# Performance work log

Measured on AMD Instinct MI355X. Metric: run time of the kernel, lower is better.

The kernel has to match this reference:

```python
import jax, jax.numpy as jnp
import numpy as np

B, C, G, N_OBJ = 256, 1019, 7, 16
IMG_SIZE = 448.0

def setup_inputs() -> dict:
    key = jax.random.key(0)
    k1, k2, k3, k4 = jax.random.split(key, 4)
    outputs = jax.random.normal(k1, (B, 5 + C, G, G), dtype=jnp.float32)
    boxes = jax.random.uniform(k2, (B, N_OBJ, 4), dtype=jnp.float32, minval=0.0, maxval=IMG_SIZE)
    labels = jax.random.randint(k3, (B, N_OBJ), 1, C + 1, dtype=jnp.int32)  # 1..C (code uses label-1)
    coords = jax.random.randint(k4, (B, N_OBJ, 2), 0, G, dtype=jnp.int32)   # (x, y) grid cells
    # objectness target matrix: 1.0 at cells containing an object, else 0 (soft CE target)
    bidx = jnp.arange(B)[:, None]
    obj = jnp.zeros((B, G, G), jnp.float32).at[bidx, coords[..., 1], coords[..., 0]].set(1.0)
    obj_matrix = obj.reshape(B, G * G)
    return {"outputs": outputs, "boxes": boxes, "labels": labels, "coords": coords, "obj_matrix": obj_matrix}

def reference(outputs, boxes, labels, coords, obj_matrix):
    Bn = outputs.shape[0]
    # objectness CE with soft targets: mean over batch of -sum(target * log_softmax(pred))
    p_obj = outputs[:, 0].reshape(Bn, -1)                      # [B, 49]
    cel_obj = jnp.mean(-jnp.sum(obj_matrix * jax.nn.log_softmax(p_obj, axis=-1), axis=-1))
    # gather per-object predictions at grid cells (x=coords[...,0], y=coords[...,1])
    bidx = jnp.arange(Bn)[:, None]
    y = coords[..., 1]
    x = coords[..., 0]
    pred_boxes = outputs[:, 1:5][bidx, :, y, x]                # [B, N_OBJ, 4]
    tgt_scaled = jnp.round(boxes / IMG_SIZE * 10.0) / 10.0     # np.round(x/IMG_SIZE, 1)
    bb_loss = jnp.sum((tgt_scaled - pred_boxes) ** 2) / Bn
    # per-object class cross-entropy, summed then divided by batch
    pred_labels = outputs[:, 5:][bidx, :, y, x]                # [B, N_OBJ, C]
    logp = jax.nn.log_softmax(pred_labels, axis=-1)
    ce = -jnp.take_along_axis(logp, (labels - 1)[..., None].astype(jnp.int32), axis=-1)
    cel_class = jnp.sum(ce) / Bn
    return cel_obj + bb_loss + cel_class
```

## Files before the change

### kernel.cpp

```cpp
#include <hip/hip_runtime.h>

#define BATCH 256
#define NCLS  1019
#define GRID  7
#define NOBJ  16
#define PLANE 49
#define NCH   1024
#define SLAB  (NCH * PLANE)
#define TPB   1024
#define NWAVE 16
#define NGRP  16

__global__ __launch_bounds__(TPB) void yolo_loss_kernel(
    const float* __restrict__ outputs,
    const float* __restrict__ boxes,
    const int*   __restrict__ labels,
    const int*   __restrict__ coords,
    const float* __restrict__ obj_matrix,
    float* __restrict__ out)
{
    const int b    = blockIdx.x;
    const int t    = threadIdx.x;
    const int lane = t & 63;
    const int w    = t >> 6;

    __shared__ float s_slot[NWAVE][4 * PLANE];
    __shared__ float s_sum[PLANE];
    __shared__ int   s_pos[NOBJ];
    __shared__ int   s_cl[NOBJ];
    __shared__ float s_red;

    const float*  ob  = outputs + (size_t)b * SLAB;
    const float4* ob4 = (const float4*)ob;

    if (t == 0) s_red = 0.0f;
    if (t < NOBJ) {
        int x = coords[(b * NOBJ + t) * 2 + 0];
        int y = coords[(b * NOBJ + t) * 2 + 1];
        s_pos[t] = y * GRID + x;
        s_cl[t]  = labels[b * NOBJ + t] - 1;
    }
    __syncthreads();

    if (w == 1) {
        float l = (lane < PLANE) ? ob[lane] : 0.0f;
        float s = (lane < PLANE) ? __expf(l) : 0.0f;
#pragma unroll
        for (int off = 32; off > 0; off >>= 1)
            s += __shfl_xor(s, off, 64);
        float lse = __logf(s);
        float mm = (lane < PLANE) ? obj_matrix[b * PLANE + lane] : 0.0f;
        float contrib = (lane < PLANE) ? -mm * (l - lse) : 0.0f;
#pragma unroll
        for (int off = 32; off > 0; off >>= 1)
            contrib += __shfl_xor(contrib, off, 64);
        if (lane == 0) atomicAdd(&s_red, contrib);
    }

    if (w == 2) {
        int o = lane >> 2, k = lane & 3;
        float pred = ob[(size_t)(1 + k) * PLANE + s_pos[o]];
        float tb   = boxes[(b * NOBJ + o) * 4 + k];
        float tgt  = rintf(tb * (10.0f / 448.0f)) * 0.1f;
        float d    = tgt - pred;
        float sq   = d * d;
#pragma unroll
        for (int off = 32; off > 0; off >>= 1)
            sq += __shfl_xor(sq, off, 64);
        if (lane == 0) atomicAdd(&s_red, sq);
    }

    const bool act = lane < PLANE;
    const int  lc  = act ? lane : 0;

    const float4* base = ob4 + (size_t)PLANE * w + lc;
    float4 v[NGRP];
#pragma unroll
    for (int i = 0; i < NGRP; ++i)
        v[i] = base[(size_t)PLANE * NWAVE * i];

    float a0 = 0.0f, a1 = 0.0f, a2 = 0.0f, a3 = 0.0f;
#pragma unroll
    for (int i = 0; i < NGRP; ++i) {
        a0 += __expf(v[i].x);
        a1 += __expf(v[i].y);
        a2 += __expf(v[i].z);
        a3 += __expf(v[i].w);
    }
    if (act) {
        float4* dst = (float4*)&s_slot[w][4 * lc];
        *dst = make_float4(a0, a1, a2, a3);
    }
    __syncthreads();

    if (w == 0 && lane < PLANE) {
        float s = 0.0f;
#pragma unroll
        for (int ww = 0; ww < NWAVE; ++ww) {
#pragma unroll
            for (int k = 0; k < 4; ++k)
                s += s_slot[ww][lane + PLANE * k];
        }
        float corr = 0.0f;
#pragma unroll
        for (int r = 0; r < 5; ++r)
            corr += __expf(ob[r * PLANE + lane]);
        s_sum[lane] = s - corr;
    }
    __syncthreads();

    if (w == 0 && lane < NOBJ) {
        float se = s_sum[s_pos[lane]];
        float tl = ob[(size_t)(5 + s_cl[lane]) * PLANE + s_pos[lane]];
        float ce = __logf(se) - tl;
        atomicAdd(&s_red, ce);
    }
    __syncthreads();

    if (t == 0) atomicAdd(out, s_red * (1.0f / (float)BATCH));
}

extern "C" void kernel_launch(void* const* d_in, const int* in_sizes, int n_in,
                              void* d_out, int out_size, void* d_ws, size_t ws_size,
                              hipStream_t stream) {
    const float* outputs    = (const float*)d_in[0];
    const float* boxes      = (const float*)d_in[1];
    const int*   labels     = (const int*)d_in[2];
    const int*   coords     = (const int*)d_in[3];
    const float* obj_matrix = (const float*)d_in[4];
    float* out = (float*)d_out;

    hipMemsetAsync(out, 0, sizeof(float), stream);
    yolo_loss_kernel<<<BATCH, TPB, 0, stream>>>(outputs, boxes, labels, coords,
                                                obj_matrix, out);
}
```

Baseline: 91.85 us.

## Split loss into two kernels, halving per-block channel work for more parallelism

The single per-batch kernel becomes two. The first kernel launches two blocks per batch item, each summing exponentials over half the channels and writing partial sums to workspace. The second kernel, small and with 128 threads, handles objectness CE, box loss and class CE using those partial sums. The memset is replaced by the first kernel zeroing the output. This doubles the block count so more CUs are busy on the 256-CU device, at the cost of a second launch and a workspace round trip.

```diff
diff --git a/kernel.cpp b/kernel.cpp
--- a/kernel.cpp
+++ b/kernel.cpp
@@ -7,73 +7,30 @@
 #define PLANE 49
 #define NCH   1024
 #define SLAB  (NCH * PLANE)
-#define TPB   1024
 #define NWAVE 16
-#define NGRP  16
+#define NGRP  8
 
-__global__ __launch_bounds__(TPB) void yolo_loss_kernel(
+__global__ __launch_bounds__(1024, 8) void yolo_sumexp_k1(
     const float* __restrict__ outputs,
-    const float* __restrict__ boxes,
-    const int*   __restrict__ labels,
-    const int*   __restrict__ coords,
-    const float* __restrict__ obj_matrix,
+    float* __restrict__ ws,
     float* __restrict__ out)
 {
-    const int b    = blockIdx.x;
+    const int blk  = blockIdx.x;
+    const int b    = blk >> 1;
+    const int h    = blk & 1;
     const int t    = threadIdx.x;
     const int lane = t & 63;
     const int w    = t >> 6;
 
+    if (blk == 0 && t == 0) out[0] = 0.0f;
+
     __shared__ float s_slot[NWAVE][4 * PLANE];
-    __shared__ float s_sum[PLANE];
-    __shared__ int   s_pos[NOBJ];
-    __shared__ int   s_cl[NOBJ];
-    __shared__ float s_red;
 
-    const float*  ob  = outputs + (size_t)b * SLAB;
-    const float4* ob4 = (const float4*)ob;
-
-    if (t == 0) s_red = 0.0f;
-    if (t < NOBJ) {
-        int x = coords[(b * NOBJ + t) * 2 + 0];
-        int y = coords[(b * NOBJ + t) * 2 + 1];
-        s_pos[t] = y * GRID + x;
-        s_cl[t]  = labels[b * NOBJ + t] - 1;
-    }
-    __syncthreads();
-
-    if (w == 1) {
-        float l = (lane < PLANE) ? ob[lane] : 0.0f;
-        float s = (lane < PLANE) ? __expf(l) : 0.0f;
-#pragma unroll
-        for (int off = 32; off > 0; off >>= 1)
-            s += __shfl_xor(s, off, 64);
-        float lse = __logf(s);
-        float mm = (lane < PLANE) ? obj_matrix[b * PLANE + lane] : 0.0f;
-        float contrib = (lane < PLANE) ? -mm * (l - lse) : 0.0f;
-#pragma unroll
-        for (int off = 32; off > 0; off >>= 1)
-            contrib += __shfl_xor(contrib, off, 64);
-        if (lane == 0) atomicAdd(&s_red, contrib);
-    }
-
-    if (w == 2) {
-        int o = lane >> 2, k = lane & 3;
-        float pred = ob[(size_t)(1 + k) * PLANE + s_pos[o]];
-        float tb   = boxes[(b * NOBJ + o) * 4 + k];
-        float tgt  = rintf(tb * (10.0f / 448.0f)) * 0.1f;
-        float d    = tgt - pred;
-        float sq   = d * d;
-#pragma unroll
-        for (int off = 32; off > 0; off >>= 1)
-            sq += __shfl_xor(sq, off, 64);
-        if (lane == 0) atomicAdd(&s_red, sq);
-    }
-
+    const float4* ob4 = (const float4*)(outputs + (size_t)b * SLAB);
     const bool act = lane < PLANE;
     const int  lc  = act ? lane : 0;
 
-    const float4* base = ob4 + (size_t)PLANE * w + lc;
+    const float4* base = ob4 + (size_t)PLANE * (h * 128 + w) + lc;
     float4 v[NGRP];
 #pragma unroll
     for (int i = 0; i < NGRP; ++i)
@@ -101,18 +58,77 @@
             for (int k = 0; k < 4; ++k)
                 s += s_slot[ww][lane + PLANE * k];
         }
-        float corr = 0.0f;
+        ws[(size_t)blk * PLANE + lane] = s;
+    }
+}
+
+__global__ __launch_bounds__(128) void yolo_loss_k2(
+    const float* __restrict__ outputs,
+    const float* __restrict__ boxes,
+    const int*   __restrict__ labels,
+    const int*   __restrict__ coords,
+    const float* __restrict__ obj_matrix,
+    const float* __restrict__ ws,
+    float* __restrict__ out)
+{
+    const int b    = blockIdx.x;
+    const int t    = threadIdx.x;
+    const int lane = t & 63;
+    const int w    = t >> 6;
+
+    __shared__ float s_red;
+    __shared__ int   s_pos[NOBJ];
+    __shared__ int   s_cl[NOBJ];
+
+    const float* ob = outputs + (size_t)b * SLAB;
+
+    if (t == 0) s_red = 0.0f;
+    if (t < NOBJ) {
+        int x = coords[(b * NOBJ + t) * 2 + 0];
+        int y = coords[(b * NOBJ + t) * 2 + 1];
+        s_pos[t] = y * GRID + x;
+        s_cl[t]  = labels[b * NOBJ + t] - 1;
+    }
+    __syncthreads();
+
+    if (w == 0) {
+        float l = (lane < PLANE) ? ob[lane] : 0.0f;
+        float s = (lane < PLANE) ? __expf(l) : 0.0f;
 #pragma unroll
-        for (int r = 0; r < 5; ++r)
-            corr += __expf(ob[r * PLANE + lane]);
-        s_sum[lane] = s - corr;
+        for (int off = 32; off > 0; off >>= 1)
+            s += __shfl_xor(s, off, 64);
+        float lse = __logf(s);
+        float mm = (lane < PLANE) ? obj_matrix[b * PLANE + lane] : 0.0f;
+        float contrib = (lane < PLANE) ? -mm * (l - lse) : 0.0f;
+#pragma unroll
+        for (int off = 32; off > 0; off >>= 1)
+            contrib += __shfl_xor(contrib, off, 64);
+        if (lane == 0) atomicAdd(&s_red, contrib);
+    }
+
+    if (w == 1) {
+        int o = lane >> 2, k = lane & 3;
+        float pred = ob[(size_t)(1 + k) * PLANE + s_pos[o]];
+        float tb   = boxes[(b * NOBJ + o) * 4 + k];
+        float tgt  = rintf(tb * (10.0f / 448.0f)) * 0.1f;
+        float d    = tgt - pred;
+        float sq   = d * d;
+#pragma unroll
+        for (int off = 32; off > 0; off >>= 1)
+            sq += __shfl_xor(sq, off, 64);
+        if (lane == 0) atomicAdd(&s_red, sq);
     }
     __syncthreads();
 
     if (w == 0 && lane < NOBJ) {
-        float se = s_sum[s_pos[lane]];
-        float tl = ob[(size_t)(5 + s_cl[lane]) * PLANE + s_pos[lane]];
-        float ce = __logf(se) - tl;
+        int p = s_pos[lane];
+        float se = ws[(size_t)(b * 2) * PLANE + p] + ws[(size_t)(b * 2 + 1) * PLANE + p];
+        float corr = 0.0f;
+#pragma unroll
+        for (int r = 0; r < 5; ++r)
+            corr += __expf(ob[r * PLANE + p]);
+        float tl = ob[(size_t)(5 + s_cl[lane]) * PLANE + p];
+        float ce = __logf(se - corr) - tl;
         atomicAdd(&s_red, ce);
     }
     __syncthreads();
@@ -129,8 +145,9 @@
     const int*   coords     = (const int*)d_in[3];
     const float* obj_matrix = (const float*)d_in[4];
     float* out = (float*)d_out;
+    float* ws  = (float*)d_ws;
 
-    hipMemsetAsync(out, 0, sizeof(float), stream);
-    yolo_loss_kernel<<<BATCH, TPB, 0, stream>>>(outputs, boxes, labels, coords,
-                                                obj_matrix, out);
+    yolo_sumexp_k1<<<BATCH * 2, 1024, 0, stream>>>(outputs, ws, out);
+    yolo_loss_k2<<<BATCH, 128, 0, stream>>>(outputs, boxes, labels, coords,
+                                            obj_matrix, ws, out);
 }
```

Result: slower. 94.45 us (+2.8%).
